# Kernel tuning notes

Hardware: AMD Instinct MI355X
Metric: run time of the kernel (lower is better)

Reference implementation:

```python
import jax, jax.numpy as jnp
import numpy as np

D = 512
HEADS, DIM_HEAD, LANDMARKS, PINV_ITERS = 8, 64, 256, 6
CONV_K = 33  # residual depthwise conv kernel over sequence dim


def _ln(x, g, b, eps=1e-5):
    mu = x.mean(-1, keepdims=True)
    var = ((x - mu) ** 2).mean(-1, keepdims=True)
    return (x - mu) / jnp.sqrt(var + eps) * g + b


def _moe(x, gw, gb, f1w, f1b, l1g, l1b, f2w, f2b, l2g, l2b, k):
    # Dense grouped-expert evaluation (same math as per-token dispatch in torch source).
    scores = x @ gw + gb                               # [B,N,E]
    topk_s, topk_i = jax.lax.top_k(scores, k)          # [B,N,k]
    h = jnp.einsum('bnd,edh->benh', x, f1w) + f1b[None, :, None, :]
    h = jax.nn.relu(_ln(h, l1g[None, :, None, :], l1b[None, :, None, :]))
    o = jnp.einsum('benh,ehd->bend', h, f2w) + f2b[None, :, None, :]
    o = _ln(o, l2g[None, :, None, :], l2b[None, :, None, :])  # [B,E,N,D]
    o = jnp.take_along_axis(jnp.swapaxes(o, 1, 2), topk_i[..., None], axis=2)  # [B,N,k,D]
    w = jax.nn.softmax(topk_s, axis=-1)[..., None]
    return (w * o).sum(axis=2) + x


def _pinv(x, iters):
    # Moore-Penrose iterative pseudoinverse (lucidrains nystrom-attention)
    col = jnp.abs(x).sum(-1).max()
    row = jnp.abs(x).sum(-2).max()
    z = jnp.swapaxes(x, -1, -2) / (col * row)
    I = jnp.eye(x.shape[-1], dtype=x.dtype)
    for _ in range(iters):
        xz = x @ z
        z = 0.25 * z @ (13 * I - xz @ (15 * I - xz @ (7 * I - xz)))
    return z


def _nystrom(x, qkv_w, out_w, out_b, conv_w):
    b, n, _ = x.shape
    m, h, dh = LANDMARKS, HEADS, DIM_HEAD
    pad = (m - n % m) % m
    x = jnp.pad(x, ((0, 0), (pad, 0), (0, 0)))  # pad at FRONT, as in source
    npd = n + pad
    qkv = x @ qkv_w                              # [b, npd, 3*h*dh]
    q, k, v = [t.reshape(b, npd, h, dh).transpose(0, 2, 1, 3) for t in jnp.split(qkv, 3, axis=-1)]
    q = q * dh ** -0.5
    l = npd // m
    q_l = q.reshape(b, h, m, l, dh).mean(3)      # landmark means
    k_l = k.reshape(b, h, m, l, dh).mean(3)
    attn1 = jax.nn.softmax(jnp.einsum('bhid,bhjd->bhij', q, k_l), -1)    # [b,h,npd,m]
    attn2 = jax.nn.softmax(jnp.einsum('bhid,bhjd->bhij', q_l, k_l), -1)  # [b,h,m,m]
    attn3 = jax.nn.softmax(jnp.einsum('bhid,bhjd->bhij', q_l, k), -1)    # [b,h,m,npd]
    out = (attn1 @ _pinv(attn2, PINV_ITERS)) @ (attn3 @ v)               # [b,h,npd,dh]
    res = jax.lax.conv_general_dilated(
        v, conv_w, (1, 1), [(CONV_K // 2, CONV_K // 2), (0, 0)],
        dimension_numbers=('NCHW', 'OIHW', 'NCHW'), feature_group_count=h)
    out = out + res
    out = out.transpose(0, 2, 1, 3).reshape(b, npd, h * dh)
    out = out @ out_w + out_b
    return out[:, -n:]


def setup_inputs() -> dict:
    key = jax.random.key(0)
    ks = iter(jax.random.split(key, 64))
    def rn(shape, s=0.02):
        return jax.random.normal(next(ks), shape, jnp.float32) * s
    inp = {'features': jax.random.normal(next(ks), (4, 6000, D), jnp.float32)}
    inp['cls_token'] = rn((1, 1, D), 1e-6)
    def moe_params(pfx, E):
        inp[pfx + '_gate_w'] = rn((D, E)); inp[pfx + '_gate_b'] = jnp.zeros((E,), jnp.float32)
        inp[pfx + '_fc1_w'] = rn((E, D, D)); inp[pfx + '_fc1_b'] = jnp.zeros((E, D), jnp.float32)
        inp[pfx + '_ln1_g'] = jnp.ones((E, D), jnp.float32); inp[pfx + '_ln1_b'] = jnp.zeros((E, D), jnp.float32)
        inp[pfx + '_fc2_w'] = rn((E, D, D)); inp[pfx + '_fc2_b'] = jnp.zeros((E, D), jnp.float32)
        inp[pfx + '_ln2_g'] = jnp.ones((E, D), jnp.float32); inp[pfx + '_ln2_b'] = jnp.zeros((E, D), jnp.float32)
    moe_params('moe1', 2)
    moe_params('moe2', 4)
    def layer_params(pfx):
        inp[pfx + '_norm_g'] = jnp.ones((D,), jnp.float32); inp[pfx + '_norm_b'] = jnp.zeros((D,), jnp.float32)
        inp[pfx + '_qkv_w'] = rn((D, 3 * HEADS * DIM_HEAD))
        inp[pfx + '_out_w'] = rn((HEADS * DIM_HEAD, D)); inp[pfx + '_out_b'] = jnp.zeros((D,), jnp.float32)
        inp[pfx + '_conv_w'] = rn((HEADS, 1, CONV_K, 1))
    layer_params('l1')
    layer_params('l2')
    return inp


def reference(features, cls_token,
              moe1_gate_w, moe1_gate_b, moe1_fc1_w, moe1_fc1_b, moe1_ln1_g, moe1_ln1_b, moe1_fc2_w, moe1_fc2_b, moe1_ln2_g, moe1_ln2_b,
              moe2_gate_w, moe2_gate_b, moe2_fc1_w, moe2_fc1_b, moe2_ln1_g, moe2_ln1_b, moe2_fc2_w, moe2_fc2_b, moe2_ln2_g, moe2_ln2_b,
              l1_norm_g, l1_norm_b, l1_qkv_w, l1_out_w, l1_out_b, l1_conv_w,
              l2_norm_g, l2_norm_b, l2_qkv_w, l2_out_w, l2_out_b, l2_conv_w):
    B, N, _ = features.shape
    _H = int(np.ceil(np.sqrt(N)))
    add = _H * _H - N
    h = jnp.concatenate([features, features[:, :add]], axis=1)      # square pad by wrap
    h = jnp.concatenate([jnp.broadcast_to(cls_token, (B, 1, D)), h], axis=1)
    h = _moe(h, moe1_gate_w, moe1_gate_b, moe1_fc1_w, moe1_fc1_b, moe1_ln1_g, moe1_ln1_b, moe1_fc2_w, moe1_fc2_b, moe1_ln2_g, moe1_ln2_b, k=1)
    h = h + _nystrom(_ln(h, l1_norm_g, l1_norm_b), l1_qkv_w, l1_out_w, l1_out_b, l1_conv_w)
    h = _moe(h, moe2_gate_w, moe2_gate_b, moe2_fc1_w, moe2_fc1_b, moe2_ln1_g, moe2_ln1_b, moe2_fc2_w, moe2_fc2_b, moe2_ln2_g, moe2_ln2_b, k=2)
    h = h + _nystrom(_ln(h, l2_norm_g, l2_norm_b), l2_qkv_w, l2_out_w, l2_out_b, l2_conv_w)
    return (h[:, 0], h[:, 1:])
```

## Files before the change

kernel.cpp:

```cpp
#include <hip/hip_runtime.h>
#include <hip/hip_bf16.h>

constexpr int BATCH = 4;
constexpr int NTOK  = 6085;
constexpr int BN_TOK = BATCH * NTOK;
constexpr int NPD   = 6144;
constexpr int RPAD  = BATCH * NPD;
constexpr int DMODEL = 512;
constexpr int NH = 8, DH = 64;
constexpr int NBH = BATCH * NH;
constexpr int LGRP = NPD / 256;
constexpr int PAD_FRONT = 59;
constexpr int CONVK = 33;
constexpr int NCH = 8;
constexpr int LISTCAP = 24576;

typedef __attribute__((ext_vector_type(8))) short short8v;
typedef __attribute__((ext_vector_type(4))) float f32x4;

__device__ __forceinline__ unsigned short f2bf(float f) {
  unsigned u = __float_as_uint(f);
  u += 0x7FFF + ((u >> 16) & 1);
  return (unsigned short)(u >> 16);
}
__device__ __forceinline__ float bf2f(unsigned short h) {
  return __uint_as_float((unsigned)h << 16);
}


__global__ void k_build_h(const float* __restrict__ feat, const float* __restrict__ cls,
                          float* __restrict__ H) {
  size_t total = (size_t)BN_TOK * DMODEL;
  for (size_t idx = (size_t)blockIdx.x * blockDim.x + threadIdx.x; idx < total;
       idx += (size_t)gridDim.x * blockDim.x) {
    int d = (int)(idx & 511);
    size_t tok = idx >> 9;
    int b = (int)(tok / NTOK), n = (int)(tok % NTOK);
    float v;
    if (n == 0) v = cls[d];
    else {
      int i = n - 1; if (i >= 6000) i -= 6000;
      v = feat[((size_t)b * 6000 + i) * DMODEL + d];
    }
    H[idx] = v;
  }
}

__global__ void k_diag_fill(float* __restrict__ out, size_t n, float val) {
  for (size_t i = (size_t)blockIdx.x * blockDim.x + threadIdx.x; i < n;
       i += (size_t)gridDim.x * blockDim.x)
    out[i] = val;
}

__global__ __launch_bounds__(256) void k_wconv(const float* __restrict__ W, int ldb,
    long long wstride, unsigned short* __restrict__ hi, unsigned short* __restrict__ lo,
    long long hstride) {
  __shared__ unsigned short Th[64][80], Tl[64][80];
  int z = blockIdx.z;
  W  += (size_t)z * (size_t)wstride;
  hi += (size_t)z * (size_t)hstride;
  lo += (size_t)z * (size_t)hstride;
  int bk = blockIdx.y * 64, bn = blockIdx.x * 64;
  int t = threadIdx.x;
  int kr = t >> 2, cq = (t & 3) * 16;
  const float* src = W + (size_t)(bk + kr) * ldb + bn + cq;
  #pragma unroll
  for (int q = 0; q < 4; ++q) {
    float4 v = *(const float4*)(src + q * 4);
    float vs[4] = {v.x, v.y, v.z, v.w};
    #pragma unroll
    for (int e = 0; e < 4; ++e) {
      int n = cq + q * 4 + e;
      unsigned short h = f2bf(vs[e]);
      Th[n][kr] = h;
      Tl[n][kr] = f2bf(vs[e] - bf2f(h));
    }
  }
  __syncthreads();
  int nr = t >> 2, kq = (t & 3) * 16;
  size_t o = (size_t)(bn + nr) * 512 + bk + kq;
  *(short8v*)&hi[o]     = *(const short8v*)&Th[nr][kq];
  *(short8v*)&hi[o + 8] = *(const short8v*)&Th[nr][kq + 8];
  *(short8v*)&lo[o]     = *(const short8v*)&Tl[nr][kq];
  *(short8v*)&lo[o + 8] = *(const short8v*)&Tl[nr][kq + 8];
}

__global__ void k_lists(const float* __restrict__ WT, int* __restrict__ cnt,
                        int* __restrict__ lists, int E) {
  int lane = threadIdx.x;
  int tok = blockIdx.x * 64 + lane;
  for (int e = 0; e < E; ++e) {
    bool sel = (tok < BN_TOK) && (WT[(size_t)tok * 4 + e] != 0.f);
    unsigned long long mask = __ballot(sel);
    int rank = __popcll(mask & ((1ull << lane) - 1ull));
    int n = __popcll(mask);
    int base = 0;
    if (lane == 0 && n > 0) base = atomicAdd(&cnt[e], n);
    base = __shfl(base, 0);
    if (sel) lists[(size_t)e * LISTCAP + base + rank] = tok;
  }
}

__global__ __launch_bounds__(256) void k_gemm_mfma(const float* __restrict__ A,
    const unsigned short* __restrict__ BtH, const unsigned short* __restrict__ BtL,
    const float* __restrict__ bias, float* __restrict__ C,
    int M, int lda, int ldc, float alpha, int omode, unsigned short* __restrict__ Clo,
    const int* __restrict__ rowidx, const int* __restrict__ cnt,
    unsigned short* __restrict__ VtH2, unsigned short* __restrict__ VtL2)
{
  __shared__ unsigned short AsH[128][40], AsL[128][40];
  __shared__ unsigned short BsH[128][40], BsL[128][40];
  int nwg = gridDim.x * gridDim.y;
  int wid = blockIdx.y * gridDim.x + blockIdx.x;
  int qq = nwg >> 3, rr = nwg & 7;
  int xcd = wid & 7, pos = wid >> 3;
  int Lid = (xcd < rr ? xcd * (qq + 1) : rr * (qq + 1) + (xcd - rr) * qq) + pos;
  int bn = (Lid % gridDim.x) * 128;
  int bm = (Lid / gridDim.x) * 128;
  int Mv = M;
  if (cnt) { Mv = *cnt; if (Mv > M) Mv = M; }
  if (bm >= Mv) return;
  int tid = threadIdx.x;
  int wave = tid >> 6, lane = tid & 63;
  int mo = (wave >> 1) * 64, no = (wave & 1) * 64;
  int r16 = lane & 15, g = lane >> 4;
  f32x4 acc[4][4] = {};
  int srow = tid >> 1, shalf = (tid & 1) * 16;
  int lrow = bm + srow;
  bool avalid = lrow < Mv;
  int arow = lrow;
  if (rowidx && avalid) arow = rowidx[lrow];
  if (!avalid) arow = 0;
  const float* aptr = A + (size_t)arow * lda + shalf;
  const unsigned short* bhptr = BtH + (size_t)(bn + srow) * 512 + shalf;
  const unsigned short* blptr = BtL + (size_t)(bn + srow) * 512 + shalf;
  for (int k0 = 0; k0 < 512; k0 += 32) {
    unsigned short h8[16], l8[16];
    #pragma unroll
    for (int q = 0; q < 4; ++q) {
      float4 v = avalid ? *(const float4*)(aptr + k0 + q * 4) : make_float4(0.f, 0.f, 0.f, 0.f);
      float vs[4] = {v.x, v.y, v.z, v.w};
      #pragma unroll
      for (int e = 0; e < 4; ++e) {
        unsigned short hh = f2bf(vs[e]);
        h8[q * 4 + e] = hh;
        l8[q * 4 + e] = f2bf(vs[e] - bf2f(hh));
      }
    }
    *(short8v*)&AsH[srow][shalf]     = *(short8v*)&h8[0];
    *(short8v*)&AsH[srow][shalf + 8] = *(short8v*)&h8[8];
    *(short8v*)&AsL[srow][shalf]     = *(short8v*)&l8[0];
    *(short8v*)&AsL[srow][shalf + 8] = *(short8v*)&l8[8];
    *(short8v*)&BsH[srow][shalf]     = *(const short8v*)(bhptr + k0);
    *(short8v*)&BsH[srow][shalf + 8] = *(const short8v*)(bhptr + k0 + 8);
    *(short8v*)&BsL[srow][shalf]     = *(const short8v*)(blptr + k0);
    *(short8v*)&BsL[srow][shalf + 8] = *(const short8v*)(blptr + k0 + 8);
    __syncthreads();
    short8v ah[4], al[4], bh[4], bl[4];
    #pragma unroll
    for (int mt = 0; mt < 4; ++mt) {
      ah[mt] = *(const short8v*)&AsH[mo + mt * 16 + r16][g * 8];
      al[mt] = *(const short8v*)&AsL[mo + mt * 16 + r16][g * 8];
    }
    #pragma unroll
    for (int nt = 0; nt < 4; ++nt) {
      bh[nt] = *(const short8v*)&BsH[no + nt * 16 + r16][g * 8];
      bl[nt] = *(const short8v*)&BsL[no + nt * 16 + r16][g * 8];
    }
    #pragma unroll
    for (int mt = 0; mt < 4; ++mt)
      #pragma unroll
      for (int nt = 0; nt < 4; ++nt) {
        acc[mt][nt] = __builtin_amdgcn_mfma_f32_16x16x32_bf16(ah[mt], bh[nt], acc[mt][nt], 0, 0, 0);
        acc[mt][nt] = __builtin_amdgcn_mfma_f32_16x16x32_bf16(ah[mt], bl[nt], acc[mt][nt], 0, 0, 0);
        acc[mt][nt] = __builtin_amdgcn_mfma_f32_16x16x32_bf16(al[mt], bh[nt], acc[mt][nt], 0, 0, 0);
      }
    __syncthreads();
  }
  #pragma unroll
  for (int mt = 0; mt < 4; ++mt)
    #pragma unroll
    for (int nt = 0; nt < 4; ++nt)
      #pragma unroll
      for (int j = 0; j < 4; ++j) {
        int lr = bm + mo + mt * 16 + g * 4 + j;
        int gc = bn + no + nt * 16 + r16;
        if (lr >= Mv) continue;
        int gr = rowidx ? rowidx[lr] : lr;
        float v = alpha * acc[mt][nt][j] + (bias ? bias[gc] : 0.f);
        if (omode == 0) {
          C[(size_t)gr * ldc + gc] = v;
        } else if (omode == 2) {
          int bb = gr / NPD, ii = gr % NPD;
          if (ii >= PAD_FRONT)
            C[((size_t)bb * NTOK + ii - PAD_FRONT) * 512 + gc] += v;
        } else if (omode == 6) {
          int bb = gr / NPD, ii = gr % NPD;
          int hh = gc >> 6, dd = gc & 63;
          size_t idx = (((size_t)bb * NH + hh) * NPD + ii) * 64 + dd;
          unsigned short hi = f2bf(v);
          ((unsigned short*)C)[idx] = hi;
          Clo[idx] = f2bf(v - bf2f(hi));
        } else {
          int bb = gr / NPD, ii = gr % NPD;
          unsigned short hi = f2bf(v);
          unsigned short lo = f2bf(v - bf2f(hi));
          if (gc < 512) {
            int hh = gc >> 6, dd = gc & 63;
            size_t idx = (((size_t)bb * NH + hh) * NPD + ii) * 64 + dd;
            ((unsigned short*)C)[idx] = hi;
            Clo[idx] = lo;
          } else {
            int gc2 = gc - 512;
            int hh = gc2 >> 6, dd = gc2 & 63;
            size_t idx = (((size_t)bb * NH + hh) * 64 + dd) * (size_t)NPD + ii;
            VtH2[idx] = hi;
            VtL2[idx] = lo;
          }
        }
      }
}

__global__ __launch_bounds__(256) void k_gemm_mfma2(const float* __restrict__ A,
    const float* __restrict__ Bt, float* __restrict__ C,
    float alpha, int omode, float cdiag, int premap, int nprod, float* __restrict__ Ct)
{
  __shared__ unsigned short AsH[128][40], AsL[128][40];
  __shared__ unsigned short BsH[128][40], BsL[128][40];
  size_t zo = (size_t)blockIdx.z * 65536;
  int bm = blockIdx.y * 128, bn = blockIdx.x * 128;
  int tid = threadIdx.x;
  int wave = tid >> 6, lane = tid & 63;
  int mo = (wave >> 1) * 64, no = (wave & 1) * 64;
  int r16 = lane & 15, g = lane >> 4;
  f32x4 acc[4][4] = {};
  int srow = tid >> 1, shalf = (tid & 1) * 16;
  int grow = bm + srow;
  int gn = bn + srow;
  for (int k0 = 0; k0 < 256; k0 += 32) {
    unsigned short h8[16], l8[16];
    #pragma unroll
    for (int q = 0; q < 4; ++q) {
      float4 v = *(const float4*)&A[zo + (size_t)grow * 256 + k0 + shalf + q * 4];
      float vs[4] = {v.x, v.y, v.z, v.w};
      #pragma unroll
      for (int e = 0; e < 4; ++e) {
        float a = vs[e];
        if (premap) a = ((grow == (k0 + shalf + q * 4 + e)) ? 7.f : 0.f) - a;
        unsigned short hh = f2bf(a);
        h8[q * 4 + e] = hh;
        l8[q * 4 + e] = (nprod == 3) ? f2bf(a - bf2f(hh)) : (unsigned short)0;
      }
    }
    *(short8v*)&AsH[srow][shalf]     = *(short8v*)&h8[0];
    *(short8v*)&AsH[srow][shalf + 8] = *(short8v*)&h8[8];
    *(short8v*)&AsL[srow][shalf]     = *(short8v*)&l8[0];
    *(short8v*)&AsL[srow][shalf + 8] = *(short8v*)&l8[8];
    #pragma unroll
    for (int q = 0; q < 4; ++q) {
      float4 v = *(const float4*)&Bt[zo + (size_t)gn * 256 + k0 + shalf + q * 4];
      float vs[4] = {v.x, v.y, v.z, v.w};
      #pragma unroll
      for (int e = 0; e < 4; ++e) {
        unsigned short hh = f2bf(vs[e]);
        h8[q * 4 + e] = hh;
        l8[q * 4 + e] = (nprod == 3) ? f2bf(vs[e] - bf2f(hh)) : (unsigned short)0;
      }
    }
    *(short8v*)&BsH[srow][shalf]     = *(short8v*)&h8[0];
    *(short8v*)&BsH[srow][shalf + 8] = *(short8v*)&h8[8];
    *(short8v*)&BsL[srow][shalf]     = *(short8v*)&l8[0];
    *(short8v*)&BsL[srow][shalf + 8] = *(short8v*)&l8[8];
    __syncthreads();
    short8v ah[4], al[4], bh[4], bl[4];
    #pragma unroll
    for (int mt = 0; mt < 4; ++mt) {
      ah[mt] = *(const short8v*)&AsH[mo + mt * 16 + r16][g * 8];
      al[mt] = *(const short8v*)&AsL[mo + mt * 16 + r16][g * 8];
    }
    #pragma unroll
    for (int nt = 0; nt < 4; ++nt) {
      bh[nt] = *(const short8v*)&BsH[no + nt * 16 + r16][g * 8];
      bl[nt] = *(const short8v*)&BsL[no + nt * 16 + r16][g * 8];
    }
    #pragma unroll
    for (int mt = 0; mt < 4; ++mt)
      #pragma unroll
      for (int nt = 0; nt < 4; ++nt) {
        acc[mt][nt] = __builtin_amdgcn_mfma_f32_16x16x32_bf16(ah[mt], bh[nt], acc[mt][nt], 0, 0, 0);
        if (nprod == 3) {
          acc[mt][nt] = __builtin_amdgcn_mfma_f32_16x16x32_bf16(ah[mt], bl[nt], acc[mt][nt], 0, 0, 0);
          acc[mt][nt] = __builtin_amdgcn_mfma_f32_16x16x32_bf16(al[mt], bh[nt], acc[mt][nt], 0, 0, 0);
        }
      }
    __syncthreads();
  }
  #pragma unroll
  for (int mt = 0; mt < 4; ++mt)
    #pragma unroll
    for (int nt = 0; nt < 4; ++nt) {
      float tv[4];
      int gr0 = bm + mo + mt * 16 + g * 4;
      int gc = bn + no + nt * 16 + r16;
      #pragma unroll
      for (int j = 0; j < 4; ++j) {
        int gr = gr0 + j;
        float v;
        if (omode == 5) v = ((gr == gc) ? cdiag : 0.f) - acc[mt][nt][j];
        else            v = alpha * acc[mt][nt][j];
        C[zo + (size_t)gr * 256 + gc] = v;
        tv[j] = v;
      }
      if (Ct) *(float4*)&Ct[zo + (size_t)gc * 256 + gr0] = *(float4*)&tv[0];
    }
}

__global__ void k_yz0(const float* __restrict__ A2, float* __restrict__ Y,
                      float* __restrict__ Z, const unsigned int* __restrict__ sc) {
  float scale = 1.f / __uint_as_float(sc[0]);
  size_t total = (size_t)NBH * 65536;
  for (size_t idx = (size_t)blockIdx.x * blockDim.x + threadIdx.x; idx < total;
       idx += (size_t)gridDim.x * blockDim.x) {
    size_t bh = idx >> 16; int r = (int)((idx >> 8) & 255); int cc = (int)(idx & 255);
    Y[idx] = A2[idx] * scale;
    Z[idx] = A2[(bh << 16) + (size_t)cc * 256 + r] * scale;
  }
}

__global__ __launch_bounds__(256) void k_gemm(const float* __restrict__ A,
    const float* __restrict__ B,
    const float* __restrict__ bias, float* __restrict__ C,
    int M, int N, int K, int lda, int ldb, int ldc,
    long long sA, long long sB, long long sC, float alpha, int omode, float cdiag)
{
  __shared__ float As[16][65];
  __shared__ float Bs[16][65];
  int z = blockIdx.z;
  A += (size_t)z * (size_t)sA;
  B += (size_t)z * (size_t)sB;
  int bm = blockIdx.y * 64, bn = blockIdx.x * 64;
  int tid = threadIdx.x;
  int tr = tid >> 4, tc = tid & 15;
  int ar = tid >> 2, aq = tid & 3;
  int br = tid >> 4, bq = tid & 15;
  float acc[4][4] = {};
  for (int k0 = 0; k0 < K; k0 += 16) {
    {
      int gr = bm + ar;
      float4 v = make_float4(0.f, 0.f, 0.f, 0.f);
      if (gr < M) v = *(const float4*)&A[(size_t)gr * lda + k0 + aq * 4];
      As[aq * 4 + 0][ar] = v.x; As[aq * 4 + 1][ar] = v.y;
      As[aq * 4 + 2][ar] = v.z; As[aq * 4 + 3][ar] = v.w;
    }
    {
      float4 v = *(const float4*)&B[(size_t)(k0 + br) * ldb + bn + bq * 4];
      Bs[br][bq * 4 + 0] = v.x; Bs[br][bq * 4 + 1] = v.y;
      Bs[br][bq * 4 + 2] = v.z; Bs[br][bq * 4 + 3] = v.w;
    }
    __syncthreads();
    #pragma unroll
    for (int kk = 0; kk < 16; ++kk) {
      float a[4], bv[4];
      #pragma unroll
      for (int i = 0; i < 4; ++i) a[i] = As[kk][tr * 4 + i];
      #pragma unroll
      for (int j = 0; j < 4; ++j) bv[j] = Bs[kk][tc * 4 + j];
      #pragma unroll
      for (int i = 0; i < 4; ++i)
        #pragma unroll
        for (int j = 0; j < 4; ++j) acc[i][j] += a[i] * bv[j];
    }
    __syncthreads();
  }
  #pragma unroll
  for (int i = 0; i < 4; ++i) {
    int gr = bm + tr * 4 + i;
    if (gr >= M) continue;
    #pragma unroll
    for (int j = 0; j < 4; ++j) {
      int gc = bn + tc * 4 + j;
      if (omode == 7) {
        float v = ((gc < 512) ? 0.125f : 1.f) * acc[i][j];
        if (gc < 512) C[(size_t)gr * 512 + gc] = v;
        else          C[524288 + (size_t)gr * 512 + (gc - 512)] = v;
      } else if (omode == 5) {
        C[(size_t)z * (size_t)sC + (size_t)gr * ldc + gc] =
            ((gr == gc) ? cdiag : 0.f) - acc[i][j];
      } else {
        C[(size_t)z * (size_t)sC + (size_t)gr * ldc + gc] =
            alpha * acc[i][j] + (bias ? bias[gc] : 0.f);
      }
    }
  }
}

__global__ void k_gate(const float* __restrict__ X, const float* __restrict__ gw,
                       const float* __restrict__ gb, float* __restrict__ WT, int E, int k) {
  int tok = blockIdx.x; int lane = threadIdx.x;
  const float* x = X + (size_t)tok * DMODEL;
  float s[4] = {0.f, 0.f, 0.f, 0.f};
  for (int d = lane; d < DMODEL; d += 64) {
    float xv = x[d];
    for (int e = 0; e < E; ++e) s[e] += xv * gw[(size_t)d * E + e];
  }
  #pragma unroll
  for (int off = 32; off; off >>= 1) {
    #pragma unroll
    for (int e = 0; e < 4; ++e) s[e] += __shfl_down(s[e], off);
  }
  if (lane == 0) {
    for (int e = 0; e < E; ++e) s[e] += gb[e];
    float w[4] = {0.f, 0.f, 0.f, 0.f};
    int i1 = 0;
    for (int e = 1; e < E; ++e) if (s[e] > s[i1]) i1 = e;
    if (k == 1) {
      w[i1] = 1.f;
    } else {
      int i2 = -1;
      for (int e = 0; e < E; ++e) { if (e == i1) continue; if (i2 < 0 || s[e] > s[i2]) i2 = e; }
      float e2 = expf(s[i2] - s[i1]);
      float zz = 1.f + e2;
      w[i1] = 1.f / zz; w[i2] = e2 / zz;
    }
    #pragma unroll
    for (int e = 0; e < 4; ++e) WT[(size_t)tok * 4 + e] = w[e];
  }
}

__device__ __forceinline__ void wave_ln_stats(const float* x, int lane, float& mu, float& rstd) {
  float s = 0.f, q = 0.f;
  #pragma unroll
  for (int j = 0; j < 8; ++j) { float v = x[lane + 64 * j]; s += v; q += v * v; }
  #pragma unroll
  for (int off = 32; off; off >>= 1) { s += __shfl_xor(s, off); q += __shfl_xor(q, off); }
  mu = s * (1.f / 512.f);
  float var = q * (1.f / 512.f) - mu * mu;
  rstd = rsqrtf(var + 1e-5f);
}

__global__ void k_ln_relu_g(float* __restrict__ T, const float* __restrict__ g,
                            const float* __restrict__ b,
                            const int* __restrict__ lists, const int* __restrict__ cnt) {
  int i = blockIdx.x;
  if (i >= *cnt) return;
  int row = lists[i];
  int lane = threadIdx.x;
  float* x = T + (size_t)row * 512;
  float mu, rstd; wave_ln_stats(x, lane, mu, rstd);
  #pragma unroll
  for (int j = 0; j < 8; ++j) {
    int d = lane + 64 * j;
    float v = (x[d] - mu) * rstd * g[d] + b[d];
    x[d] = fmaxf(v, 0.f);
  }
}

__global__ void k_ln_waccum(const float* __restrict__ T, float* __restrict__ H,
                            const float* __restrict__ g, const float* __restrict__ b,
                            const float* __restrict__ WT, int e) {
  int row = blockIdx.x;
  float w = WT[(size_t)row * 4 + e];
  if (w == 0.f) return;
  int lane = threadIdx.x;
  const float* x = T + (size_t)row * 512;
  float mu, rstd; wave_ln_stats(x, lane, mu, rstd);
  float* h = H + (size_t)row * 512;
  #pragma unroll
  for (int j = 0; j < 8; ++j) {
    int d = lane + 64 * j;
    h[d] += w * ((x[d] - mu) * rstd * g[d] + b[d]);
  }
}

__global__ __launch_bounds__(256) void k_ln_pad_mean(const float* __restrict__ H,
    float* __restrict__ XLn, float* __restrict__ Xm,
    const float* __restrict__ g, const float* __restrict__ b) {
  int z = blockIdx.x;
  int bb = z >> 8, jm = z & 255;
  int wave = threadIdx.x >> 6, lane = threadIdx.x & 63;
  __shared__ float part[4][512];
  float racc[8] = {};
  for (int t6 = 0; t6 < 6; ++t6) {
    int t = wave * 6 + t6;
    int i = jm * LGRP + t;
    float* y = XLn + ((size_t)bb * NPD + i) * 512;
    if (i < PAD_FRONT) {
      #pragma unroll
      for (int j = 0; j < 8; ++j) y[lane + 64 * j] = 0.f;
      continue;
    }
    const float* x = H + ((size_t)bb * NTOK + (i - PAD_FRONT)) * 512;
    float vals[8];
    #pragma unroll
    for (int j = 0; j < 8; ++j) vals[j] = x[lane + 64 * j];
    float s = 0.f, q = 0.f;
    #pragma unroll
    for (int j = 0; j < 8; ++j) { s += vals[j]; q += vals[j] * vals[j]; }
    #pragma unroll
    for (int off = 32; off; off >>= 1) { s += __shfl_xor(s, off); q += __shfl_xor(q, off); }
    float mu = s * (1.f / 512.f);
    float rstd = rsqrtf(q * (1.f / 512.f) - mu * mu + 1e-5f);
    #pragma unroll
    for (int j = 0; j < 8; ++j) {
      int d = lane + 64 * j;
      float v = (vals[j] - mu) * rstd * g[d] + b[d];
      y[d] = v;
      racc[j] += v;
    }
  }
  #pragma unroll
  for (int j = 0; j < 8; ++j) part[wave][lane + 64 * j] = racc[j];
  __syncthreads();
  for (int c = threadIdx.x; c < 512; c += 256) {
    float s = part[0][c] + part[1][c] + part[2][c] + part[3][c];
    Xm[(size_t)z * 512 + c] = s * (1.f / LGRP);
  }
}

__global__ __launch_bounds__(256) void k_colmax(const float* __restrict__ A2,
                                                unsigned int* __restrict__ sc) {
  int bh = blockIdx.x; int t = threadIdx.x;
  const float* A = A2 + (size_t)bh * 65536;
  float colsum = 0.f;
  for (int jj = 0; jj < 256; ++jj) colsum += fabsf(A[(size_t)jj * 256 + t]);
  __shared__ float sh[256];
  sh[t] = colsum; __syncthreads();
  for (int s = 128; s; s >>= 1) { if (t < s) sh[t] = fmaxf(sh[t], sh[t + s]); __syncthreads(); }
  if (t == 0) atomicMax(&sc[0], __float_as_uint(sh[0]));
}

__global__ __launch_bounds__(256) void k_attn2(const float* __restrict__ QL,
                                               const float* __restrict__ KL,
                                               float* __restrict__ A2) {
  int z = blockIdx.x; int bh = z >> 8, j = z & 255;
  int b = bh >> 3, h = bh & 7;
  int t = threadIdx.x;
  __shared__ float q[64]; __shared__ float red[256];
  __shared__ float mshare, sshare;
  if (t < 64) q[t] = QL[((size_t)b * 256 + j) * 512 + h * 64 + t];
  __syncthreads();
  const float* kl = KL + ((size_t)b * 256 + t) * 512 + h * 64;
  float s = 0.f;
  #pragma unroll
  for (int d = 0; d < 64; ++d) s += q[d] * kl[d];
  red[t] = s; __syncthreads();
  for (int st = 128; st; st >>= 1) { if (t < st) red[t] = fmaxf(red[t], red[t + st]); __syncthreads(); }
  if (t == 0) mshare = red[0];
  __syncthreads();
  float e = expf(s - mshare);
  red[t] = e; __syncthreads();
  for (int st = 128; st; st >>= 1) { if (t < st) red[t] += red[t + st]; __syncthreads(); }
  if (t == 0) sshare = red[0];
  __syncthreads();
  A2[((size_t)bh * 256 + j) * 256 + t] = e / sshare;
}

__global__ void k_cvt_kl(const float* __restrict__ KL, unsigned short* __restrict__ KH,
                         unsigned short* __restrict__ KLo) {
  int idx = blockIdx.x * 256 + threadIdx.x;
  int bh = idx >> 14, j = (idx >> 6) & 255, d = idx & 63;
  int b = bh >> 3, h = bh & 7;
  float v = KL[((size_t)b * 256 + j) * 512 + h * 64 + d];
  unsigned short hi = f2bf(v);
  KH[idx] = hi; KLo[idx] = f2bf(v - bf2f(hi));
}

__global__ void k_cvt_w2t(const float* __restrict__ W2b, unsigned short* __restrict__ WH,
                          unsigned short* __restrict__ WL) {
  int idx = blockIdx.x * 256 + threadIdx.x;
  int bh = idx >> 14, d = (idx >> 8) & 63, j = idx & 255;
  float v = W2b[((size_t)bh * 256 + j) * 64 + d];
  unsigned short hi = f2bf(v);
  WH[idx] = hi; WL[idx] = f2bf(v - bf2f(hi));
}

__global__ __launch_bounds__(256) void k_flash_pre(
    const float* __restrict__ Qp, long long Qsb, long long Qsh, int Qsr,
    const unsigned short* __restrict__ KHg, const unsigned short* __restrict__ KLg,
    long long Ksbh,
    const unsigned short* __restrict__ VtHg, const unsigned short* __restrict__ VtLg,
    long long Vsbh, int Vrow,
    float* __restrict__ Op, long long Osb, long long Osh, int Osr,
    float* __restrict__ Opart, float* __restrict__ ML,
    int tiles_per_chunk, int mode)
{
  int jt = blockIdx.x, bh = blockIdx.y, ch = blockIdx.z;
  int b = bh >> 3, h = bh & 7;
  const float* Qb = Qp + (size_t)b * Qsb + (size_t)h * Qsh;
  const unsigned short* KbH = KHg + (size_t)bh * Ksbh;
  const unsigned short* KbL = KLg + (size_t)bh * Ksbh;
  const unsigned short* VbH = VtHg + (size_t)bh * Vsbh;
  const unsigned short* VbL = VtLg + (size_t)bh * Vsbh;
  int tid = threadIdx.x;
  int wave = tid >> 6, lane = tid & 63;
  int r16 = lane & 15, g = lane >> 4;
  int q0 = jt * 64 + wave * 16;

  __shared__ unsigned short KsH[64][72], KsL[64][72];
  __shared__ unsigned short VtH[64][72], VtL[64][72];

  short8v qh[2], ql[2];
  #pragma unroll
  for (int kk = 0; kk < 2; ++kk) {
    const float* qr = Qb + (size_t)(q0 + r16) * Qsr + kk * 32 + g * 8;
    float4 v0 = *(const float4*)qr;
    float4 v1 = *(const float4*)(qr + 4);
    float vs[8] = {v0.x, v0.y, v0.z, v0.w, v1.x, v1.y, v1.z, v1.w};
    unsigned short hh[8], llo[8];
    #pragma unroll
    for (int e = 0; e < 8; ++e) {
      hh[e] = f2bf(vs[e]); llo[e] = f2bf(vs[e] - bf2f(hh[e]));
    }
    qh[kk] = *(short8v*)&hh[0];
    ql[kk] = *(short8v*)&llo[0];
  }

  f32x4 O4[4] = {};
  float m[4], lsum[4];
  #pragma unroll
  for (int j = 0; j < 4; ++j) { m[j] = -1e30f; lsum[j] = 0.f; }

  int t0 = ch * tiles_per_chunk;
  for (int tt = t0; tt < t0 + tiles_per_chunk; ++tt) {
    int key0 = tt * 64;
    __syncthreads();
    {
      const unsigned short* ksrcH = KbH + (size_t)key0 * 64;
      const unsigned short* ksrcL = KbL + (size_t)key0 * 64;
      #pragma unroll
      for (int u = 0; u < 2; ++u) {
        int idx = tid + 256 * u;
        int r = idx >> 3, c8 = (idx & 7) * 8;
        *(short8v*)&KsH[r][c8] = *(const short8v*)&ksrcH[idx * 8];
        *(short8v*)&KsL[r][c8] = *(const short8v*)&ksrcL[idx * 8];
      }
      const unsigned short* vsrcH = VbH + key0;
      const unsigned short* vsrcL = VbL + key0;
      #pragma unroll
      for (int u = 0; u < 2; ++u) {
        int idx = tid + 256 * u;
        int d = idx >> 3, c8 = (idx & 7) * 8;
        *(short8v*)&VtH[d][c8] = *(const short8v*)&vsrcH[(size_t)d * Vrow + c8];
        *(short8v*)&VtL[d][c8] = *(const short8v*)&vsrcL[(size_t)d * Vrow + c8];
      }
    }
    __syncthreads();
    f32x4 S[4] = {};
    #pragma unroll
    for (int kk = 0; kk < 2; ++kk)
      #pragma unroll
      for (int nt = 0; nt < 4; ++nt) {
        short8v kh = *(const short8v*)&KsH[nt * 16 + r16][kk * 32 + g * 8];
        short8v kl = *(const short8v*)&KsL[nt * 16 + r16][kk * 32 + g * 8];
        S[nt] = __builtin_amdgcn_mfma_f32_16x16x32_bf16(qh[kk], kh, S[nt], 0, 0, 0);
        S[nt] = __builtin_amdgcn_mfma_f32_16x16x32_bf16(qh[kk], kl, S[nt], 0, 0, 0);
        S[nt] = __builtin_amdgcn_mfma_f32_16x16x32_bf16(ql[kk], kh, S[nt], 0, 0, 0);
// ... 51 lines not shown
    #pragma unroll
    for (int j = 0; j < 4; ++j) inv[j] = 1.f / lsum[j];
    #pragma unroll
    for (int nt = 0; nt < 4; ++nt)
      #pragma unroll
      for (int j = 0; j < 4; ++j)
        Ob[(size_t)(q0 + g * 4 + j) * Osr + nt * 16 + r16] = O4[nt][j] * inv[j];
  } else {
    #pragma unroll
    for (int j = 0; j < 4; ++j) {
      size_t rowbase = ((size_t)ch * NBH + bh) * 256 + q0 + g * 4 + j;
      #pragma unroll
      for (int nt = 0; nt < 4; ++nt)
        Opart[rowbase * 64 + nt * 16 + r16] = O4[nt][j];
      if (r16 == 0) { ML[rowbase * 2] = m[j]; ML[rowbase * 2 + 1] = lsum[j]; }
    }
  }
}

__global__ __launch_bounds__(256) void k_flash_comb(const float* __restrict__ Opart,
                                                    const float* __restrict__ ML,
                                                    float* __restrict__ A3V) {
  int jt = blockIdx.x, bh = blockIdx.y;
  int t = threadIdx.x;
  int jr = t >> 4, q16 = t & 15;
  int row = jt * 16 + jr;
  float mv[NCH], lv[NCH];
  float M = -1e30f;
  #pragma unroll
  for (int ch = 0; ch < NCH; ++ch) {
    size_t base = (((size_t)ch * NBH + bh) * 256 + row);
    mv[ch] = ML[base * 2]; lv[ch] = ML[base * 2 + 1];
    M = fmaxf(M, mv[ch]);
  }
  float L = 0.f;
  float4 O = make_float4(0.f, 0.f, 0.f, 0.f);
  #pragma unroll
  for (int ch = 0; ch < NCH; ++ch) {
    float c = expf(mv[ch] - M);
    L += c * lv[ch];
    size_t base = (((size_t)ch * NBH + bh) * 256 + row);
    float4 o = *(const float4*)&Opart[base * 64 + q16 * 4];
    O.x += c * o.x; O.y += c * o.y; O.z += c * o.z; O.w += c * o.w;
  }
  float inv = 1.f / L;
  *(float4*)&A3V[((size_t)bh * 256 + row) * 64 + q16 * 4] =
      make_float4(O.x * inv, O.y * inv, O.z * inv, O.w * inv);
}

__global__ __launch_bounds__(256) void k_conv_add(const unsigned short* __restrict__ VtHg,
    const unsigned short* __restrict__ VtLg, const float* __restrict__ cw,
    float* __restrict__ out) {
  int it = blockIdx.x, bh = blockIdx.y;
  int b = bh >> 3, h = bh & 7;
  int i0 = it * 128;
  int t = threadIdx.x;
  __shared__ float Vs[64][161];
  const unsigned short* vh = VtHg + (size_t)bh * 64 * NPD;
  const unsigned short* vl = VtLg + (size_t)bh * 64 * NPD;
  for (int u = 0; u < 40; ++u) {
    int idx = t + 256 * u;
    int d = idx / 160, ii = idx - d * 160;
    int gi = i0 - 16 + ii;
    float v = 0.f;
    if (gi >= 0 && gi < NPD) {
      size_t a = (size_t)d * NPD + gi;
      v = bf2f(vh[a]) + bf2f(vl[a]);
    }
    Vs[d][ii] = v;
  }
  __syncthreads();
  float w[CONVK];
  #pragma unroll
  for (int p = 0; p < CONVK; ++p) w[p] = cw[h * CONVK + p];
  int rgrp = t >> 6, d = t & 63;
  for (int r = rgrp * 32; r < rgrp * 32 + 32; ++r) {
    float acc = 0.f;
    #pragma unroll
    for (int p = 0; p < CONVK; ++p) acc += w[p] * Vs[d][r + p];
    out[((size_t)b * NPD + i0 + r) * 512 + h * 64 + d] += acc;
  }
}

__global__ void k_out_write(const float* __restrict__ H, float* __restrict__ out) {
  size_t n0 = (size_t)BATCH * 512;
  size_t total = n0 + (size_t)BATCH * (NTOK - 1) * 512;
  for (size_t idx = (size_t)blockIdx.x * blockDim.x + threadIdx.x; idx < total;
       idx += (size_t)gridDim.x * blockDim.x) {
    float v;
    if (idx < n0) {
      int b = (int)(idx >> 9); int d = (int)(idx & 511);
      v = H[((size_t)b * NTOK) * 512 + d];
    } else {
      size_t r = idx - n0;
      size_t bj = r >> 9; int d = (int)(r & 511);
      int b = (int)(bj / (NTOK - 1)); int j = (int)(bj % (NTOK - 1));
      v = H[((size_t)b * NTOK + 1 + j) * 512 + d];
    }
    out[idx] = v;
  }
}


extern "C" void kernel_launch(void* const* d_in, const int* in_sizes, int n_in,
                              void* d_out, int out_size, void* d_ws, size_t ws_size,
                              hipStream_t stream) {
  (void)in_sizes; (void)n_in;

  const float* feat = (const float*)d_in[0];
  const float* cls  = (const float*)d_in[1];
  const float* m1_gw = (const float*)d_in[2];  const float* m1_gb = (const float*)d_in[3];
  const float* m1_f1w = (const float*)d_in[4]; const float* m1_f1b = (const float*)d_in[5];
  const float* m1_l1g = (const float*)d_in[6]; const float* m1_l1b = (const float*)d_in[7];
  const float* m1_f2w = (const float*)d_in[8]; const float* m1_f2b = (const float*)d_in[9];
  const float* m1_l2g = (const float*)d_in[10]; const float* m1_l2b = (const float*)d_in[11];
  const float* m2_gw = (const float*)d_in[12]; const float* m2_gb = (const float*)d_in[13];
  const float* m2_f1w = (const float*)d_in[14]; const float* m2_f1b = (const float*)d_in[15];
  const float* m2_l1g = (const float*)d_in[16]; const float* m2_l1b = (const float*)d_in[17];
  const float* m2_f2w = (const float*)d_in[18]; const float* m2_f2b = (const float*)d_in[19];
  const float* m2_l2g = (const float*)d_in[20]; const float* m2_l2b = (const float*)d_in[21];
  const float* l1_ng = (const float*)d_in[22]; const float* l1_nb = (const float*)d_in[23];
  const float* l1_qkvw = (const float*)d_in[24]; const float* l1_outw = (const float*)d_in[25];
  const float* l1_outb = (const float*)d_in[26]; const float* l1_convw = (const float*)d_in[27];
  const float* l2_ng = (const float*)d_in[28]; const float* l2_nb = (const float*)d_in[29];
  const float* l2_qkvw = (const float*)d_in[30]; const float* l2_outw = (const float*)d_in[31];
  const float* l2_outb = (const float*)d_in[32]; const float* l2_convw = (const float*)d_in[33];

  constexpr size_t SZ_H    = (size_t)BN_TOK * 512;
  constexpr size_t SZ_ROW  = (size_t)RPAD * 512;
  float* W = (float*)d_ws;
  float* H  = W;
  float* WT = W + SZ_H;
  unsigned int* SC = (unsigned int*)(W + SZ_H + 97360);
  float* pool = W + SZ_H + 97360 + 16;

  float* R2 = pool;
  float* R3 = pool + SZ_ROW;
  float* R4 = pool + 2 * SZ_ROW;
  float* SMALL = pool + 3 * SZ_ROW;
  float* Xm  = SMALL;
  float* QL  = SMALL + 524288;
  float* KL  = SMALL + 1048576;
  float* A2  = SMALL + 1572864;
  float* Zb  = SMALL + 3670016;
  float* XZp = SMALL + 5767168;
  float* Wa  = SMALL + 7864320;
  float* Wb  = SMALL + 9961472;
  float* A3V = SMALL + 12058624;
  float* W2b = SMALL + 12582912;
  size_t total_f = (SZ_H + 97360 + 16) + 3 * SZ_ROW + 13107200;
  if (total_f * 4 > ws_size) {
    k_diag_fill<<<2048, 256, 0, stream>>>((float*)d_out, (size_t)out_size,
                                          (float)(ws_size >> 20));
    return;
  }

  k_build_h<<<2048, 256, 0, stream>>>(feat, cls, H);

  auto run_moe = [&](const float* gw, const float* gb, const float* f1w, const float* f1b,
                     const float* l1g, const float* l1b, const float* f2w, const float* f2b,
                     const float* l2g, const float* l2b, int E, int k) {
    float* T1 = R2; float* T2 = R3; float* Xsnap = R4;
    unsigned short* BtF1H = (unsigned short*)A2;
    unsigned short* BtF1L = BtF1H + (size_t)E * 262144;
    unsigned short* BtF2H = (unsigned short*)(A2 + 1048576);
    unsigned short* BtF2L = BtF2H + (size_t)E * 262144;
    int* LISTS = (int*)Zb;
    int* CNT = (int*)(SC + 4);
    hipMemcpyAsync(Xsnap, H, SZ_H * 4, hipMemcpyDeviceToDevice, stream);
    hipMemsetAsync(CNT, 0, 4 * sizeof(int), stream);
    k_gate<<<BN_TOK, 64, 0, stream>>>(H, gw, gb, WT, E, k);
    k_lists<<<(BN_TOK + 63) / 64, 64, 0, stream>>>(WT, CNT, LISTS, E);
    k_wconv<<<dim3(8, 8, E), 256, 0, stream>>>(f1w, 512, 262144LL, BtF1H, BtF1L, 262144LL);
    k_wconv<<<dim3(8, 8, E), 256, 0, stream>>>(f2w, 512, 262144LL, BtF2H, BtF2L, 262144LL);
    dim3 g(4, (BN_TOK + 127) / 128, 1);
    for (int e = 0; e < E; ++e) {
      const int* lst = LISTS + (size_t)e * LISTCAP;
      const int* cnt = CNT + e;
      k_gemm_mfma<<<g, 256, 0, stream>>>(Xsnap, BtF1H + (size_t)e * 262144,
          BtF1L + (size_t)e * 262144, f1b + e * 512, T1,
          BN_TOK, 512, 512, 1.f, 0, nullptr, lst, cnt, nullptr, nullptr);
      k_ln_relu_g<<<BN_TOK, 64, 0, stream>>>(T1, l1g + e * 512, l1b + e * 512, lst, cnt);
      k_gemm_mfma<<<g, 256, 0, stream>>>(T1, BtF2H + (size_t)e * 262144,
          BtF2L + (size_t)e * 262144, f2b + e * 512, T2,
          BN_TOK, 512, 512, 1.f, 0, nullptr, lst, cnt, nullptr, nullptr);
      k_ln_waccum<<<BN_TOK, 64, 0, stream>>>(T2, H, l2g + e * 512, l2b + e * 512, WT, e);
    }
  };

  auto run_attn = [&](const float* ng, const float* nb, const float* qkvw, const float* outw,
                      const float* outb, const float* convw) {
    float* XLn = R2; float* AttnO = R2;
    float* Qb = R3;
    unsigned short* KH  = (unsigned short*)R3;
    unsigned short* KLo = KH + 12582912;
    unsigned short* VtH = (unsigned short*)R4;
    unsigned short* VtL = VtH + 12582912;
    k_ln_pad_mean<<<BATCH * 256, 256, 0, stream>>>(H, XLn, Xm, ng, nb);
    k_gemm<<<dim3(16, 16, 1), 256, 0, stream>>>(Xm, qkvw, nullptr, QL,
        1024, 1024, 512, 512, 1536, 512, 0, 0, 0, 1.f, 7, 0.f);
    k_attn2<<<NBH * 256, 256, 0, stream>>>(QL, KL, A2);
    hipMemsetAsync(SC, 0, 8, stream);
    k_colmax<<<NBH, 256, 0, stream>>>(A2, SC);
    k_yz0<<<2048, 256, 0, stream>>>(A2, Zb, Wb, SC);
    float* Y = Zb; float* Z = Wb; float* F1 = XZp; float* F2 = Wa;
    dim3 gq(2, 2, NBH);
    for (int it = 0; it < 6; ++it) {
      int np = (it < 4) ? 1 : 3;
      k_gemm_mfma2<<<gq, 256, 0, stream>>>(A2, Y, F1, 1.f, 0, 0.f, 0, np, F2);
      k_gemm_mfma2<<<gq, 256, 0, stream>>>(F2, F1, Y, 1.f, 5, 15.f, 1, np, nullptr);
      k_gemm_mfma2<<<gq, 256, 0, stream>>>(Y, F1, F2, 1.f, 5, 13.f, 0, np, nullptr);
      k_gemm_mfma2<<<gq, 256, 0, stream>>>(Z, F2, F1, 0.25f, 0, 0.f, 0, np, Y);
      float* tz = Z; Z = F1; F1 = tz;
    }
    unsigned short* KLH = (unsigned short*)A2;
    unsigned short* KLL = KLH + 524288;
    unsigned short* W2tH = KLH + 1048576;
    unsigned short* W2tL = KLH + 1572864;
    k_cvt_kl<<<2048, 256, 0, stream>>>(KL, KLH, KLL);
    unsigned short* BtQH = (unsigned short*)Wa;
    unsigned short* BtQL = BtQH + 786432;
    k_wconv<<<dim3(24, 8, 1), 256, 0, stream>>>(qkvw, 1536, 0LL, BtQH, BtQL, 0LL);
    dim3 gr(4, (RPAD + 127) / 128, 1);
    k_gemm_mfma<<<dim3(8, (RPAD + 127) / 128, 1), 256, 0, stream>>>(
        XLn, BtQH + 512 * 512, BtQL + 512 * 512, nullptr,
        (float*)KH, RPAD, 512, 512, 1.f, 8, KLo, nullptr, nullptr, VtH, VtL);
    k_flash_pre<<<dim3(4, NBH, NCH), 256, 0, stream>>>(
        QL, 131072LL, 64LL, 512,
        KH, KLo, (long long)NPD * 64,
        VtH, VtL, (long long)64 * NPD, NPD,
        nullptr, 0, 0, 0, Zb, Xm, NPD / (64 * NCH), 1);
    k_flash_comb<<<dim3(16, NBH), 256, 0, stream>>>(Zb, Xm, A3V);
    k_gemm<<<dim3(1, 4, NBH), 256, 0, stream>>>(Z, A3V, nullptr, W2b,
        256, 64, 256, 256, 64, 64, 65536, 16384, 16384, 1.f, 0, 0.f);
    k_cvt_w2t<<<2048, 256, 0, stream>>>(W2b, W2tH, W2tL);
    k_gemm_mfma<<<gr, 256, 0, stream>>>(XLn, BtQH, BtQL, nullptr,
        Qb, RPAD, 512, 512, 0.125f, 0, nullptr, nullptr, nullptr, nullptr, nullptr);
    k_flash_pre<<<dim3(NPD / 64, NBH, 1), 256, 0, stream>>>(
        Qb, (long long)NPD * 512, 64LL, 512,
        KLH, KLL, 16384LL,
        W2tH, W2tL, 16384LL, 256,
        AttnO, (long long)NPD * 512, 64LL, 512,
        nullptr, nullptr, 4, 0);
    k_conv_add<<<dim3(NPD / 128, NBH), 256, 0, stream>>>(VtH, VtL, convw, AttnO);
    unsigned short* BtOH = (unsigned short*)Wa;
    unsigned short* BtOL = BtOH + 262144;
    k_wconv<<<dim3(8, 8, 1), 256, 0, stream>>>(outw, 512, 0LL, BtOH, BtOL, 0LL);
    k_gemm_mfma<<<gr, 256, 0, stream>>>(AttnO, BtOH, BtOL, outb,
        H, RPAD, 512, 512, 1.f, 2, nullptr, nullptr, nullptr, nullptr, nullptr);
  };

  run_moe(m1_gw, m1_gb, m1_f1w, m1_f1b, m1_l1g, m1_l1b, m1_f2w, m1_f2b, m1_l2g, m1_l2b, 2, 1);
  run_attn(l1_ng, l1_nb, l1_qkvw, l1_outw, l1_outb, l1_convw);
  run_moe(m2_gw, m2_gb, m2_f1w, m2_f1b, m2_l1g, m2_l1b, m2_f2w, m2_f2b, m2_l2g, m2_l2b, 4, 2);
  run_attn(l2_ng, l2_nb, l2_qkvw, l2_outw, l2_outb, l2_convw);

  k_out_write<<<2048, 256, 0, stream>>>(H, (float*)d_out);
}
```

Before: 3.607 ms.

## Fuse output write, W2 transpose, memsets, and coalesce V-transpose stores

The V-transpose epilogue of the QKV GEMM now goes through a shared-memory tile, so the hi/lo bf16 stores along the sequence dimension are coalesced instead of strided scatters. The final output-copy kernel is folded into the last out-projection GEMM epilogue, and the W2 hi/lo transpose conversion is folded into the small fp32 GEMM. The memsets for the expert counters and the scale word are moved into the first kernels of each stage. Together these remove several launches and a full pass over the hidden state, at the cost of more complex epilogues and an extra LDS round trip.

```diff
diff --git a/kernel.cpp b/kernel.cpp
--- a/kernel.cpp
+++ b/kernel.cpp
@@ -106,10 +106,14 @@
     const float* __restrict__ bias, float* __restrict__ C,
     int M, int lda, int ldc, float alpha, int omode, unsigned short* __restrict__ Clo,
     const int* __restrict__ rowidx, const int* __restrict__ cnt,
-    unsigned short* __restrict__ VtH2, unsigned short* __restrict__ VtL2)
+    unsigned short* __restrict__ VtH2, unsigned short* __restrict__ VtL2,
+    float* __restrict__ Out2)
 {
-  __shared__ unsigned short AsH[128][40], AsL[128][40];
-  __shared__ unsigned short BsH[128][40], BsL[128][40];
+  __shared__ alignas(16) unsigned short SMEM[20480];
+  auto AsH = (unsigned short(*)[40])(SMEM + 0);
+  auto AsL = (unsigned short(*)[40])(SMEM + 5120);
+  auto BsH = (unsigned short(*)[40])(SMEM + 10240);
+  auto BsL = (unsigned short(*)[40])(SMEM + 15360);
   int nwg = gridDim.x * gridDim.y;
   int wid = blockIdx.y * gridDim.x + blockIdx.x;
   int qq = nwg >> 3, rr = nwg & 7;
@@ -177,6 +181,39 @@
       }
     __syncthreads();
   }
+  if (omode == 8 && bn >= 512) {
+    auto VT = (unsigned short(*)[130])(SMEM);
+    int bb = bm / NPD, ii0 = bm % NPD;
+    int gc2base = bn - 512;
+    for (int pass = 0; pass < 2; ++pass) {
+      __syncthreads();
+      #pragma unroll
+      for (int mt = 0; mt < 4; ++mt)
+        #pragma unroll
+        for (int nt = 0; nt < 4; ++nt)
+          #pragma unroll
+          for (int j = 0; j < 4; ++j) {
+            int rl = mo + mt * 16 + g * 4 + j;
+            int cl = no + nt * 16 + r16;
+            float v = alpha * acc[mt][nt][j];
+            unsigned short hi = f2bf(v);
+            VT[cl][rl] = pass ? f2bf(v - bf2f(hi)) : hi;
+          }
+      __syncthreads();
+      unsigned short* dst = pass ? VtL2 : VtH2;
+      for (int u = 0; u < 32; ++u) {
+        int row = u * 4 + (tid >> 6);
+        int cp = tid & 63;
+        int gc2 = gc2base + row;
+        int hh = gc2 >> 6, dd = gc2 & 63;
+        size_t base = (((size_t)bb * NH + hh) * 64 + dd) * (size_t)NPD + ii0 + cp * 2;
+        unsigned int val = (unsigned int)VT[row][cp * 2] |
+                           ((unsigned int)VT[row][cp * 2 + 1] << 16);
+        *(unsigned int*)&dst[base] = val;
+      }
+    }
+    return;
+  }
   #pragma unroll
   for (int mt = 0; mt < 4; ++mt)
     #pragma unroll
@@ -194,29 +231,24 @@
           int bb = gr / NPD, ii = gr % NPD;
           if (ii >= PAD_FRONT)
             C[((size_t)bb * NTOK + ii - PAD_FRONT) * 512 + gc] += v;
-        } else if (omode == 6) {
+        } else if (omode == 9) {
+          int bb = gr / NPD, ii = gr % NPD;
+          if (ii >= PAD_FRONT) {
+            int n = ii - PAD_FRONT;
+            size_t hidx = ((size_t)bb * NTOK + n) * 512 + gc;
+            float hv = C[hidx] + v;
+            C[hidx] = hv;
+            if (n == 0) Out2[(size_t)bb * 512 + gc] = hv;
+            else Out2[(size_t)BATCH * 512 +
+                      ((size_t)bb * (NTOK - 1) + (n - 1)) * 512 + gc] = hv;
+          }
+        } else {
           int bb = gr / NPD, ii = gr % NPD;
           int hh = gc >> 6, dd = gc & 63;
           size_t idx = (((size_t)bb * NH + hh) * NPD + ii) * 64 + dd;
           unsigned short hi = f2bf(v);
           ((unsigned short*)C)[idx] = hi;
           Clo[idx] = f2bf(v - bf2f(hi));
-        } else {
-          int bb = gr / NPD, ii = gr % NPD;
-          unsigned short hi = f2bf(v);
-          unsigned short lo = f2bf(v - bf2f(hi));
-          if (gc < 512) {
-            int hh = gc >> 6, dd = gc & 63;
-            size_t idx = (((size_t)bb * NH + hh) * NPD + ii) * 64 + dd;
-            ((unsigned short*)C)[idx] = hi;
-            Clo[idx] = lo;
-          } else {
-            int gc2 = gc - 512;
-            int hh = gc2 >> 6, dd = gc2 & 63;
-            size_t idx = (((size_t)bb * NH + hh) * 64 + dd) * (size_t)NPD + ii;
-            VtH2[idx] = hi;
-            VtL2[idx] = lo;
-          }
         }
       }
 }
@@ -331,7 +363,8 @@
     const float* __restrict__ B,
     const float* __restrict__ bias, float* __restrict__ C,
     int M, int N, int K, int lda, int ldb, int ldc,
-    long long sA, long long sB, long long sC, float alpha, int omode, float cdiag)
+    long long sA, long long sB, long long sC, float alpha, int omode, float cdiag,
+    unsigned short* __restrict__ TH, unsigned short* __restrict__ TL)
 {
   __shared__ float As[16][65];
   __shared__ float Bs[16][65];
@@ -383,6 +416,13 @@
         float v = ((gc < 512) ? 0.125f : 1.f) * acc[i][j];
         if (gc < 512) C[(size_t)gr * 512 + gc] = v;
         else          C[524288 + (size_t)gr * 512 + (gc - 512)] = v;
+      } else if (omode == 10) {
+        float v = alpha * acc[i][j];
+        C[(size_t)z * (size_t)sC + (size_t)gr * ldc + gc] = v;
+        size_t tidx = ((size_t)z * 64 + gc) * 256 + gr;
+        unsigned short hi = f2bf(v);
+        TH[tidx] = hi;
+        TL[tidx] = f2bf(v - bf2f(hi));
       } else if (omode == 5) {
         C[(size_t)z * (size_t)sC + (size_t)gr * ldc + gc] =
             ((gr == gc) ? cdiag : 0.f) - acc[i][j];
@@ -395,8 +435,10 @@
 }
 
 __global__ void k_gate(const float* __restrict__ X, const float* __restrict__ gw,
-                       const float* __restrict__ gb, float* __restrict__ WT, int E, int k) {
+                       const float* __restrict__ gb, float* __restrict__ WT, int E, int k,
+                       int* __restrict__ CNT) {
   int tok = blockIdx.x; int lane = threadIdx.x;
+  if (blockIdx.x == 0 && lane < 4) CNT[lane] = 0;
   const float* x = X + (size_t)tok * DMODEL;
   float s[4] = {0.f, 0.f, 0.f, 0.f};
   for (int d = lane; d < DMODEL; d += 64) {
@@ -474,8 +516,10 @@
 
 __global__ __launch_bounds__(256) void k_ln_pad_mean(const float* __restrict__ H,
     float* __restrict__ XLn, float* __restrict__ Xm,
-    const float* __restrict__ g, const float* __restrict__ b) {
+    const float* __restrict__ g, const float* __restrict__ b,
+    unsigned int* __restrict__ sc) {
   int z = blockIdx.x;
+  if (z == 0 && threadIdx.x == 0) sc[0] = 0u;
   int bb = z >> 8, jm = z & 255;
   int wave = threadIdx.x >> 6, lane = threadIdx.x & 63;
   __shared__ float part[4][512];
@@ -563,15 +607,6 @@
   float v = KL[((size_t)b * 256 + j) * 512 + h * 64 + d];
   unsigned short hi = f2bf(v);
   KH[idx] = hi; KLo[idx] = f2bf(v - bf2f(hi));
-}
-
-__global__ void k_cvt_w2t(const float* __restrict__ W2b, unsigned short* __restrict__ WH,
-                          unsigned short* __restrict__ WL) {
-  int idx = blockIdx.x * 256 + threadIdx.x;
-  int bh = idx >> 14, d = (idx >> 8) & 63, j = idx & 255;
-  float v = W2b[((size_t)bh * 256 + j) * 64 + d];
-  unsigned short hi = f2bf(v);
-  WH[idx] = hi; WL[idx] = f2bf(v - bf2f(hi));
 }
 
 __global__ __launch_bounds__(256) void k_flash_pre(
@@ -789,25 +824,6 @@
   }
 }
 
-__global__ void k_out_write(const float* __restrict__ H, float* __restrict__ out) {
-  size_t n0 = (size_t)BATCH * 512;
-  size_t total = n0 + (size_t)BATCH * (NTOK - 1) * 512;
-  for (size_t idx = (size_t)blockIdx.x * blockDim.x + threadIdx.x; idx < total;
-       idx += (size_t)gridDim.x * blockDim.x) {
-    float v;
-    if (idx < n0) {
-      int b = (int)(idx >> 9); int d = (int)(idx & 511);
-      v = H[((size_t)b * NTOK) * 512 + d];
-    } else {
-      size_t r = idx - n0;
-      size_t bj = r >> 9; int d = (int)(r & 511);
-      int b = (int)(bj / (NTOK - 1)); int j = (int)(bj % (NTOK - 1));
-      v = H[((size_t)b * NTOK + 1 + j) * 512 + d];
-    }
-    out[idx] = v;
-  }
-}
-
 
 extern "C" void kernel_launch(void* const* d_in, const int* in_sizes, int n_in,
                               void* d_out, int out_size, void* d_ws, size_t ws_size,
@@ -875,8 +891,7 @@
     int* LISTS = (int*)Zb;
     int* CNT = (int*)(SC + 4);
     hipMemcpyAsync(Xsnap, H, SZ_H * 4, hipMemcpyDeviceToDevice, stream);
-    hipMemsetAsync(CNT, 0, 4 * sizeof(int), stream);
-    k_gate<<<BN_TOK, 64, 0, stream>>>(H, gw, gb, WT, E, k);
+    k_gate<<<BN_TOK, 64, 0, stream>>>(H, gw, gb, WT, E, k, CNT);
     k_lists<<<(BN_TOK + 63) / 64, 64, 0, stream>>>(WT, CNT, LISTS, E);
     k_wconv<<<dim3(8, 8, E), 256, 0, stream>>>(f1w, 512, 262144LL, BtF1H, BtF1L, 262144LL);
     k_wconv<<<dim3(8, 8, E), 256, 0, stream>>>(f2w, 512, 262144LL, BtF2H, BtF2L, 262144LL);
@@ -886,28 +901,27 @@
       const int* cnt = CNT + e;
       k_gemm_mfma<<<g, 256, 0, stream>>>(Xsnap, BtF1H + (size_t)e * 262144,
           BtF1L + (size_t)e * 262144, f1b + e * 512, T1,
-          BN_TOK, 512, 512, 1.f, 0, nullptr, lst, cnt, nullptr, nullptr);
+          BN_TOK, 512, 512, 1.f, 0, nullptr, lst, cnt, nullptr, nullptr, nullptr);
       k_ln_relu_g<<<BN_TOK, 64, 0, stream>>>(T1, l1g + e * 512, l1b + e * 512, lst, cnt);
       k_gemm_mfma<<<g, 256, 0, stream>>>(T1, BtF2H + (size_t)e * 262144,
           BtF2L + (size_t)e * 262144, f2b + e * 512, T2,
-          BN_TOK, 512, 512, 1.f, 0, nullptr, lst, cnt, nullptr, nullptr);
+          BN_TOK, 512, 512, 1.f, 0, nullptr, lst, cnt, nullptr, nullptr, nullptr);
       k_ln_waccum<<<BN_TOK, 64, 0, stream>>>(T2, H, l2g + e * 512, l2b + e * 512, WT, e);
     }
   };
 
   auto run_attn = [&](const float* ng, const float* nb, const float* qkvw, const float* outw,
-                      const float* outb, const float* convw) {
+                      const float* outb, const float* convw, float* outp) {
     float* XLn = R2; float* AttnO = R2;
     float* Qb = R3;
     unsigned short* KH  = (unsigned short*)R3;
     unsigned short* KLo = KH + 12582912;
     unsigned short* VtH = (unsigned short*)R4;
     unsigned short* VtL = VtH + 12582912;
-    k_ln_pad_mean<<<BATCH * 256, 256, 0, stream>>>(H, XLn, Xm, ng, nb);
+    k_ln_pad_mean<<<BATCH * 256, 256, 0, stream>>>(H, XLn, Xm, ng, nb, SC);
     k_gemm<<<dim3(16, 16, 1), 256, 0, stream>>>(Xm, qkvw, nullptr, QL,
-        1024, 1024, 512, 512, 1536, 512, 0, 0, 0, 1.f, 7, 0.f);
+        1024, 1024, 512, 512, 1536, 512, 0, 0, 0, 1.f, 7, 0.f, nullptr, nullptr);
     k_attn2<<<NBH * 256, 256, 0, stream>>>(QL, KL, A2);
-    hipMemsetAsync(SC, 0, 8, stream);
     k_colmax<<<NBH, 256, 0, stream>>>(A2, SC);
     k_yz0<<<2048, 256, 0, stream>>>(A2, Zb, Wb, SC);
     float* Y = Zb; float* Z = Wb; float* F1 = XZp; float* F2 = Wa;
@@ -931,7 +945,7 @@
     dim3 gr(4, (RPAD + 127) / 128, 1);
     k_gemm_mfma<<<dim3(8, (RPAD + 127) / 128, 1), 256, 0, stream>>>(
         XLn, BtQH + 512 * 512, BtQL + 512 * 512, nullptr,
-        (float*)KH, RPAD, 512, 512, 1.f, 8, KLo, nullptr, nullptr, VtH, VtL);
+        (float*)KH, RPAD, 512, 512, 1.f, 8, KLo, nullptr, nullptr, VtH, VtL, nullptr);
     k_flash_pre<<<dim3(4, NBH, NCH), 256, 0, stream>>>(
         QL, 131072LL, 64LL, 512,
         KH, KLo, (long long)NPD * 64,
@@ -939,10 +953,9 @@
         nullptr, 0, 0, 0, Zb, Xm, NPD / (64 * NCH), 1);
     k_flash_comb<<<dim3(16, NBH), 256, 0, stream>>>(Zb, Xm, A3V);
     k_gemm<<<dim3(1, 4, NBH), 256, 0, stream>>>(Z, A3V, nullptr, W2b,
-        256, 64, 256, 256, 64, 64, 65536, 16384, 16384, 1.f, 0, 0.f);
-    k_cvt_w2t<<<2048, 256, 0, stream>>>(W2b, W2tH, W2tL);
+        256, 64, 256, 256, 64, 64, 65536, 16384, 16384, 1.f, 10, 0.f, W2tH, W2tL);
     k_gemm_mfma<<<gr, 256, 0, stream>>>(XLn, BtQH, BtQL, nullptr,
-        Qb, RPAD, 512, 512, 0.125f, 0, nullptr, nullptr, nullptr, nullptr, nullptr);
+        Qb, RPAD, 512, 512, 0.125f, 0, nullptr, nullptr, nullptr, nullptr, nullptr, nullptr);
     k_flash_pre<<<dim3(NPD / 64, NBH, 1), 256, 0, stream>>>(
         Qb, (long long)NPD * 512, 64LL, 512,
         KLH, KLL, 16384LL,
@@ -954,13 +967,12 @@
     unsigned short* BtOL = BtOH + 262144;
     k_wconv<<<dim3(8, 8, 1), 256, 0, stream>>>(outw, 512, 0LL, BtOH, BtOL, 0LL);
     k_gemm_mfma<<<gr, 256, 0, stream>>>(AttnO, BtOH, BtOL, outb,
-        H, RPAD, 512, 512, 1.f, 2, nullptr, nullptr, nullptr, nullptr, nullptr);
+        H, RPAD, 512, 512, 1.f, outp ? 9 : 2, nullptr, nullptr, nullptr,
+        nullptr, nullptr, outp);
   };
 
   run_moe(m1_gw, m1_gb, m1_f1w, m1_f1b, m1_l1g, m1_l1b, m1_f2w, m1_f2b, m1_l2g, m1_l2b, 2, 1);
-  run_attn(l1_ng, l1_nb, l1_qkvw, l1_outw, l1_outb, l1_convw);
+  run_attn(l1_ng, l1_nb, l1_qkvw, l1_outw, l1_outb, l1_convw, nullptr);
   run_moe(m2_gw, m2_gb, m2_f1w, m2_f1b, m2_l1g, m2_l1b, m2_f2w, m2_f2b, m2_l2g, m2_l2b, 4, 2);
-  run_attn(l2_ng, l2_nb, l2_qkvw, l2_outw, l2_outb, l2_convw);
-
-  k_out_write<<<2048, 256, 0, stream>>>(H, (float*)d_out);
-}
+  run_attn(l2_ng, l2_nb, l2_qkvw, l2_outw, l2_outb, l2_convw, (float*)d_out);
+}
```

Result: slower. 4.784 ms (+32.6%).
